# Performance work log

Measured on AMD Instinct MI355X. Metric: run time of the kernel, lower is better.

## Reference

```python
import jax, jax.numpy as jnp
import numpy as np

NUM_BINS = 256
HIST_MIN = -1.0
HIST_MAX = 1.0
EPS = 1e-8


def _histc(x, bins=NUM_BINS, lo=HIST_MIN, hi=HIST_MAX):
    # Faithful to torch.histc: values outside [lo, hi] are ignored;
    # value == hi falls into the last bin.
    x = x.reshape(-1)
    width = (hi - lo) / bins
    idx = jnp.clip(jnp.floor((x - lo) / width).astype(jnp.int32), 0, bins - 1)
    in_range = ((x >= lo) & (x <= hi)).astype(jnp.float32)
    return jax.ops.segment_sum(in_range, idx, num_segments=bins)


def _entropy(hist):
    prob = hist / jnp.sum(hist) + EPS
    return -jnp.sum(prob * jnp.log(prob))


def setup_inputs() -> dict:
    key = jax.random.key(0)
    k1, k2 = jax.random.split(key)
    shape = (64, 2, 512, 512)
    predicted_ab = jax.random.normal(k1, shape, dtype=jnp.float32)
    ground_truth_ab = jax.random.normal(k2, shape, dtype=jnp.float32)
    return {"predicted_ab": predicted_ab, "ground_truth_ab": ground_truth_ab}


def reference(predicted_ab, ground_truth_ab):
    pred_hist = _histc(predicted_ab)
    gt_hist = _histc(ground_truth_ab)
    return jnp.abs(_entropy(pred_hist) - _entropy(gt_hist))
```

## Files before the change

kernel.cpp:

```cpp
#include <hip/hip_runtime.h>
#include <math.h>

#define NBINS 256
#define NCOPY 16

__global__ __launch_bounds__(256) void hist2_kernel(const float* __restrict__ a,
                                                    const float* __restrict__ b,
                                                    unsigned int* __restrict__ ghist,
                                                    int n4a, int n4b, int half_blocks) {
    __shared__ unsigned int lh[NBINS * NCOPY];
    const int tid = threadIdx.x;
    for (int i = tid; i < NBINS * NCOPY; i += 256) lh[i] = 0u;
    __syncthreads();

    const int which = (blockIdx.x >= half_blocks) ? 1 : 0;
    const float4* __restrict__ x4 = (const float4*)(which ? b : a);
    const int n4 = which ? n4b : n4a;
    const int bid = which ? (blockIdx.x - half_blocks) : blockIdx.x;
    const int c = tid & (NCOPY - 1);
    const int stride = half_blocks * 256;

    for (int i = bid * 256 + tid; i < n4; i += stride) {
        float4 v = x4[i];
        float vv[4] = {v.x, v.y, v.z, v.w};
#pragma unroll
        for (int j = 0; j < 4; j++) {
            float f = vv[j];
            if (f >= -1.0f && f <= 1.0f) {
                int bin = (int)((f + 1.0f) * 128.0f);
                bin = bin > (NBINS - 1) ? (NBINS - 1) : bin;
                atomicAdd(&lh[(bin << 4) + c], 1u);
            }
        }
    }
    __syncthreads();

    unsigned int s = 0;
#pragma unroll
    for (int k = 0; k < NCOPY; k++) s += lh[(tid << 4) + k];
    atomicAdd(&ghist[which * NBINS + tid], s);
}

__global__ __launch_bounds__(256) void entropy_kernel(const unsigned int* __restrict__ gh,
                                                      float* __restrict__ out) {
    __shared__ double sd[NBINS];
    const int tid = threadIdx.x;
    double e[2];

    for (int h = 0; h < 2; h++) {
        const double hv = (double)gh[h * NBINS + tid];

        sd[tid] = hv;
        __syncthreads();
        for (int o = 128; o > 0; o >>= 1) {
            if (tid < o) sd[tid] += sd[tid + o];
            __syncthreads();
        }
        const double total = sd[0];
        __syncthreads();

        const double p = hv / total + 1e-8;
        sd[tid] = -p * log(p);
        __syncthreads();
        for (int o = 128; o > 0; o >>= 1) {
            if (tid < o) sd[tid] += sd[tid + o];
            __syncthreads();
        }
        e[h] = sd[0];
        __syncthreads();
    }

    if (tid == 0) out[0] = (float)fabs(e[0] - e[1]);
}

extern "C" void kernel_launch(void* const* d_in, const int* in_sizes, int n_in,
                              void* d_out, int out_size, void* d_ws, size_t ws_size,
                              hipStream_t stream) {
    const float* pred = (const float*)d_in[0];
    const float* gt   = (const float*)d_in[1];
    const int n0 = in_sizes[0];
    const int n1 = in_sizes[1];

    unsigned int* hist = (unsigned int*)d_ws;
    hipMemsetAsync(d_ws, 0, 2 * NBINS * sizeof(unsigned int), stream);

    const int half_blocks = 1024;
    hist2_kernel<<<2 * half_blocks, 256, 0, stream>>>(pred, gt, hist,
                                                      n0 / 4, n1 / 4, half_blocks);
    entropy_kernel<<<1, 256, 0, stream>>>(hist, (float*)d_out);
}
```

Before: 282.1 us.

## Replace shared atomics with per-lane private 16-bit LDS histograms

The shared histogram becomes one 16-bit sub-histogram per lane, with bins interleaved across lanes, so increments are plain LDS read-modify-writes instead of atomics. Blocks shrink to a single 64-thread wave and the grid is reduced. The main loop issues eight float4 loads before binning them, to keep more memory requests in flight, and a scalar tail loop handles leftover elements. The costs are 32KB of LDS per block, which limits resident waves per CU, and a 16-bit counter that could overflow if a single lane ever received more than 65535 samples in one bin.

```diff
diff --git a/kernel.cpp b/kernel.cpp
--- a/kernel.cpp
+++ b/kernel.cpp
@@ -2,43 +2,76 @@
 #include <math.h>
 
 #define NBINS 256
-#define NCOPY 16
 
-__global__ __launch_bounds__(256) void hist2_kernel(const float* __restrict__ a,
-                                                    const float* __restrict__ b,
-                                                    unsigned int* __restrict__ ghist,
-                                                    int n4a, int n4b, int half_blocks) {
-    __shared__ unsigned int lh[NBINS * NCOPY];
-    const int tid = threadIdx.x;
-    for (int i = tid; i < NBINS * NCOPY; i += 256) lh[i] = 0u;
+__global__ __launch_bounds__(64) void hist2_kernel(const float* __restrict__ a,
+                                                   const float* __restrict__ b,
+                                                   unsigned int* __restrict__ ghist,
+                                                   int n4a, int n4b, int na, int nb,
+                                                   int half_blocks) {
+    __shared__ unsigned short lh[NBINS * 64];
+    const int lane = threadIdx.x;
+
+    uint4* z = (uint4*)lh;
+#pragma unroll
+    for (int k = 0; k < 32; k++) z[lane + 64 * k] = make_uint4(0u, 0u, 0u, 0u);
     __syncthreads();
 
     const int which = (blockIdx.x >= half_blocks) ? 1 : 0;
     const float4* __restrict__ x4 = (const float4*)(which ? b : a);
+    const float* __restrict__ x1 = which ? b : a;
     const int n4 = which ? n4b : n4a;
+    const int n = which ? nb : na;
     const int bid = which ? (blockIdx.x - half_blocks) : blockIdx.x;
-    const int c = tid & (NCOPY - 1);
-    const int stride = half_blocks * 256;
+    const int stride = half_blocks * 64;
 
-    for (int i = bid * 256 + tid; i < n4; i += stride) {
+#define BIN1(f)                                              \
+    do {                                                     \
+        float _f = (f);                                      \
+        if (_f >= -1.0f && _f <= 1.0f) {                     \
+            int _bin = (int)((_f + 1.0f) * 128.0f);          \
+            _bin = _bin > (NBINS - 1) ? (NBINS - 1) : _bin;  \
+            int _idx = (_bin << 6) + lane;                   \
+            lh[_idx] = (unsigned short)(lh[_idx] + 1);       \
+        }                                                    \
+    } while (0)
+
+#define BIN4(v) do { BIN1((v).x); BIN1((v).y); BIN1((v).z); BIN1((v).w); } while (0)
+
+    int i = bid * 64 + lane;
+    for (; i + 7 * stride < n4; i += 8 * stride) {
+        float4 v0 = x4[i];
+        float4 v1 = x4[i + stride];
+        float4 v2 = x4[i + 2 * stride];
+        float4 v3 = x4[i + 3 * stride];
+        float4 v4 = x4[i + 4 * stride];
+        float4 v5 = x4[i + 5 * stride];
+        float4 v6 = x4[i + 6 * stride];
+        float4 v7 = x4[i + 7 * stride];
+        BIN4(v0); BIN4(v1); BIN4(v2); BIN4(v3);
+        BIN4(v4); BIN4(v5); BIN4(v6); BIN4(v7);
+    }
+    for (; i < n4; i += stride) {
         float4 v = x4[i];
-        float vv[4] = {v.x, v.y, v.z, v.w};
-#pragma unroll
-        for (int j = 0; j < 4; j++) {
-            float f = vv[j];
-            if (f >= -1.0f && f <= 1.0f) {
-                int bin = (int)((f + 1.0f) * 128.0f);
-                bin = bin > (NBINS - 1) ? (NBINS - 1) : bin;
-                atomicAdd(&lh[(bin << 4) + c], 1u);
-            }
-        }
+        BIN4(v);
     }
+    for (int t = n4 * 4 + bid * 64 + lane; t < n; t += stride) BIN1(x1[t]);
+
     __syncthreads();
 
-    unsigned int s = 0;
+    const unsigned int* lhd = (const unsigned int*)lh;
 #pragma unroll
-    for (int k = 0; k < NCOPY; k++) s += lh[(tid << 4) + k];
-    atomicAdd(&ghist[which * NBINS + tid], s);
+    for (int k = 0; k < 4; k++) {
+        const int bin = lane + (k << 6);
+        unsigned int lo = 0, hi = 0;
+#pragma unroll
+        for (int jj = 0; jj < 32; jj++) {
+            const int j = (jj + lane) & 31;
+            const unsigned int v = lhd[(bin << 5) + j];
+            lo += v & 0xFFFFu;
+            hi += v >> 16;
+        }
+        atomicAdd(&ghist[(which << 8) + bin], lo + hi);
+    }
 }
 
 __global__ __launch_bounds__(256) void entropy_kernel(const unsigned int* __restrict__ gh,
@@ -84,8 +117,9 @@
     unsigned int* hist = (unsigned int*)d_ws;
     hipMemsetAsync(d_ws, 0, 2 * NBINS * sizeof(unsigned int), stream);
 
-    const int half_blocks = 1024;
-    hist2_kernel<<<2 * half_blocks, 256, 0, stream>>>(pred, gt, hist,
-                                                      n0 / 4, n1 / 4, half_blocks);
+    const int half_blocks = 640;
+    hist2_kernel<<<2 * half_blocks, 64, 0, stream>>>(pred, gt, hist,
+                                                     n0 / 4, n1 / 4, n0, n1,
+                                                     half_blocks);
     entropy_kernel<<<1, 256, 0, stream>>>(hist, (float*)d_out);
 }
```

After: 336.3 us. +19.2%, slower.
